# Performance work log

Measured on AMD Instinct MI355X. Metric: run time of the kernel, lower is better.

Reference implementation:

```python
import jax, jax.numpy as jnp
import numpy as np

N_NODES = 100000
N_EDGES = 1200000
IN_DIM = 256
HID = 64


def _spmm(rows, cols, vals, M):
    # sparse (COO) @ dense: gather source rows, scale by edge vals, scatter-add to dest
    gathered = M[cols] * vals[:, None]          # [E, d]
    return jax.ops.segment_sum(gathered, rows, num_segments=N_NODES)


def _gcn_embed(rows, cols, vals, X, W1, b1, W2, b2):
    # layer 1: SELU(A @ (X W1) + b1)
    Z = _spmm(rows, cols, vals, X @ W1) + b1
    Z = jax.nn.selu(Z)
    # layer 2: A @ (Z W2) + b2 (no activation)
    Z = _spmm(rows, cols, vals, Z @ W2) + b2
    # row-wise L2 normalize (F.normalize, p=2, dim=1)
    norm = jnp.sqrt(jnp.sum(Z * Z, axis=1, keepdims=True))
    return Z / jnp.maximum(norm, 1e-12)


def setup_inputs() -> dict:
    key = jax.random.key(0)
    ks = jax.random.split(key, 10)
    X1 = jax.random.normal(ks[0], (N_NODES, IN_DIM), dtype=jnp.float32)
    X2 = jax.random.normal(ks[1], (N_NODES, IN_DIM), dtype=jnp.float32)
    rows1 = jax.random.randint(ks[2], (N_EDGES,), 0, N_NODES, dtype=jnp.int32)
    cols1 = jax.random.randint(ks[3], (N_EDGES,), 0, N_NODES, dtype=jnp.int32)
    vals1 = jax.random.uniform(ks[4], (N_EDGES,), dtype=jnp.float32)
    rows2 = jax.random.randint(ks[5], (N_EDGES,), 0, N_NODES, dtype=jnp.int32)
    cols2 = jax.random.randint(ks[6], (N_EDGES,), 0, N_NODES, dtype=jnp.int32)
    vals2 = jax.random.uniform(ks[7], (N_EDGES,), dtype=jnp.float32)
    # Xavier-uniform weights, zero biases (reset_parameters)
    lim1 = float(np.sqrt(6.0 / (IN_DIM + HID)))
    lim2 = float(np.sqrt(6.0 / (HID + HID)))
    W1 = jax.random.uniform(ks[8], (IN_DIM, HID), dtype=jnp.float32, minval=-lim1, maxval=lim1)
    W2 = jax.random.uniform(ks[9], (HID, HID), dtype=jnp.float32, minval=-lim2, maxval=lim2)
    b1 = jnp.zeros((HID,), dtype=jnp.float32)
    b2 = jnp.zeros((HID,), dtype=jnp.float32)
    return {"X1": X1, "X2": X2, "rows1": rows1, "cols1": cols1, "vals1": vals1,
            "rows2": rows2, "cols2": cols2, "vals2": vals2,
            "W1": W1, "b1": b1, "W2": W2, "b2": b2}


def reference(X1, X2, rows1, cols1, vals1, rows2, cols2, vals2, W1, b1, W2, b2):
    Z1 = _gcn_embed(rows1, cols1, vals1, X1, W1, b1, W2, b2)
    Z2 = _gcn_embed(rows2, cols2, vals2, X2, W1, b1, W2, b2)
    return (Z1, Z2)
```

## Files before the change

kernel.cpp:

```cpp
#include <hip/hip_runtime.h>
#include <hip/hip_bf16.h>


#define RPB 512
#define EPB 4096
#define MAXB 8192

typedef __attribute__((ext_vector_type(8))) short short8;
typedef __attribute__((ext_vector_type(4))) short short4v;
typedef __attribute__((ext_vector_type(4))) float f32x4;

__device__ __forceinline__ float selu_f(float x) {
    const float scale = 1.0507009873554805f;
    const float alpha = 1.6732632423543772f;
    return x > 0.0f ? scale * x : scale * alpha * (__expf(x) - 1.0f);
}

__device__ __forceinline__ short f2bf(float x) {
    unsigned u = __float_as_uint(x);
    u += 0x7FFF + ((u >> 16) & 1);
    return (short)(u >> 16);
}
__device__ __forceinline__ float bf2f(short h) {
    return __uint_as_float(((unsigned)(unsigned short)h) << 16);
}

__global__ void scan_a(const int* __restrict__ counts, int* __restrict__ offs,
                       int* __restrict__ partials, int N) {
    __shared__ int sh[256];
    int tid = threadIdx.x;
    int base = blockIdx.x * 1024 + tid * 4;
    int4 c = make_int4(0, 0, 0, 0);
    if (base + 3 < N) {
        c = *(const int4*)(counts + base);
    } else {
        if (base + 0 < N) c.x = counts[base + 0];
        if (base + 1 < N) c.y = counts[base + 1];
        if (base + 2 < N) c.z = counts[base + 2];
        if (base + 3 < N) c.w = counts[base + 3];
    }
    int tsum = c.x + c.y + c.z + c.w;
    sh[tid] = tsum;
    __syncthreads();
    int val = tsum;
    for (int d = 1; d < 256; d <<= 1) {
        int t = (tid >= d) ? sh[tid - d] : 0;
        __syncthreads();
        val += t;
        sh[tid] = val;
        __syncthreads();
    }
    int excl = val - tsum;
    int4 o;
    o.x = excl; o.y = o.x + c.x; o.z = o.y + c.y; o.w = o.z + c.z;
    if (base + 3 < N) {
        *(int4*)(offs + base) = o;
    } else {
        if (base + 0 < N) offs[base + 0] = o.x;
        if (base + 1 < N) offs[base + 1] = o.y;
        if (base + 2 < N) offs[base + 2] = o.z;
        if (base + 3 < N) offs[base + 3] = o.w;
    }
    if (tid == 255) partials[blockIdx.x] = val;
}

__global__ void scan_b(int* __restrict__ partials, int nb) {
    __shared__ int sh[128];
    int tid = threadIdx.x;
    int v = (tid < nb) ? partials[tid] : 0;
    sh[tid] = v;
    __syncthreads();
    int val = v;
    for (int d = 1; d < 128; d <<= 1) {
        int t = (tid >= d) ? sh[tid - d] : 0;
        __syncthreads();
        val += t;
        sh[tid] = val;
        __syncthreads();
    }
    if (tid < nb) partials[tid] = val - v;
}

__global__ void scan_c(int* __restrict__ offs, const int* __restrict__ partials,
                       int N, int E) {
    int tid = threadIdx.x;
    int base = blockIdx.x * 1024 + tid * 4;
    int add = partials[blockIdx.x];
    if (base + 3 < N) {
        int4 o = *(int4*)(offs + base);
        o.x += add; o.y += add; o.z += add; o.w += add;
        *(int4*)(offs + base) = o;
    } else {
        for (int t = 0; t < 4; t++)
            if (base + t < N) offs[base + t] += add;
    }
    if (blockIdx.x == 0 && tid == 0) offs[N] = E;
}

__global__ __launch_bounds__(256) void bucket_hist(const int* __restrict__ rows,
                                                   int* __restrict__ cntT,
                                                   int E, int nbA, int NB) {
    __shared__ int cnt[256];
    int tid = threadIdx.x;
    cnt[tid] = 0;
    __syncthreads();
    int e0 = blockIdx.x * EPB;
#pragma unroll
    for (int k = 0; k < EPB / 256; k++) {
        int e = e0 + k * 256 + tid;
        if (e < E) atomicAdd(&cnt[rows[e] >> 9], 1);
    }
    __syncthreads();
    if (tid < NB) cntT[tid * nbA + blockIdx.x] = cnt[tid];
}

__global__ __launch_bounds__(256) void coarse_scatter(const int* __restrict__ rows,
                                                      const int* __restrict__ cols,
                                                      const float* __restrict__ vals,
                                                      const int* __restrict__ csOffs,
                                                      int2* __restrict__ ecvA,
                                                      int E, int nbA, int NB) {
    __shared__ int cnt[256];
    __shared__ int loc[256];
    __shared__ int gof[256];
    __shared__ int dstBase[EPB];
    __shared__ int2 eLDS[EPB];
    int tid = threadIdx.x, blk = blockIdx.x;
    int e0 = blk * EPB;
    cnt[tid] = 0;
    __syncthreads();
#pragma unroll
    for (int k = 0; k < EPB / 256; k++) {
        int e = e0 + k * 256 + tid;
        if (e < E) atomicAdd(&cnt[rows[e] >> 9], 1);
    }
    __syncthreads();
    int my = cnt[tid];
    loc[tid] = my;
    __syncthreads();
    int val = my;
    for (int d = 1; d < 256; d <<= 1) {
        int t = (tid >= d) ? loc[tid - d] : 0;
        __syncthreads();
        val += t;
        loc[tid] = val;
        __syncthreads();
    }
    int excl = val - my;
    loc[tid] = excl;
    cnt[tid] = excl;
    gof[tid] = (tid < NB) ? csOffs[tid * nbA + blk] : 0;
    __syncthreads();
#pragma unroll
    for (int k = 0; k < EPB / 256; k++) {
        int e = e0 + k * 256 + tid;
        if (e < E) {
            int r = rows[e];
            int b = r >> 9;
            int p = atomicAdd(&cnt[b], 1);
            eLDS[p] = make_int2(((r & (RPB - 1)) << 17) | cols[e],
                                __float_as_int(vals[e]));
            dstBase[p] = gof[b] - loc[b];
        }
    }
    __syncthreads();
    int nE = min(EPB, E - e0);
    for (int j = tid; j < nE; j += 256)
        ecvA[dstBase[j] + j] = eLDS[j];
}

__global__ __launch_bounds__(256) void fine_sort(const int* __restrict__ csOffs,
                                                 const int2* __restrict__ ecvA,
                                                 int2* __restrict__ ecv,
                                                 int* __restrict__ offs,
                                                 int nbA, int N, int E) {
    __shared__ int rcnt[RPB], roff[RPB], rcur[RPB];
    __shared__ int sh[256];
    __shared__ int2 eLDS[MAXB];
    int b = blockIdx.x, tid = threadIdx.x;
    int bs = csOffs[b * nbA];
    int be = csOffs[(b + 1) * nbA];
    int cntE = be - bs;
    if (cntE > MAXB) cntE = MAXB;
    rcnt[tid] = 0;
    rcnt[tid + 256] = 0;
    __syncthreads();
    for (int j = tid; j < cntE; j += 256)
        atomicAdd(&rcnt[ecvA[bs + j].x >> 17], 1);
    __syncthreads();
    int a0 = rcnt[2 * tid], a1 = rcnt[2 * tid + 1];
    int ps = a0 + a1;
    sh[tid] = ps;
    __syncthreads();
    int val = ps;
    for (int d = 1; d < 256; d <<= 1) {
        int t = (tid >= d) ? sh[tid - d] : 0;
        __syncthreads();
        val += t;
        sh[tid] = val;
        __syncthreads();
    }
    int exclPair = val - ps;
    roff[2 * tid] = exclPair;
    roff[2 * tid + 1] = exclPair + a0;
    rcur[2 * tid] = exclPair;
    rcur[2 * tid + 1] = exclPair + a0;
    __syncthreads();
    int row0 = b * RPB;
    for (int t2 = tid; t2 < RPB; t2 += 256) {
        int row = row0 + t2;
        if (row <= N) offs[row] = bs + roff[t2];
    }
    if (b == 0 && tid == 0) offs[N] = E;
    for (int j = tid; j < cntE; j += 256) {
        int2 p = ecvA[bs + j];
        int pos = atomicAdd(&rcur[p.x >> 17], 1);
        if (pos < MAXB) eLDS[pos] = make_int2(p.x & 0x1FFFF, p.y);
    }
    __syncthreads();
    for (int j = tid; j < cntE; j += 256)
        ecv[bs + j] = eLDS[j];
}

__global__ void prep_w(const float* __restrict__ W, short* __restrict__ th,
                       short* __restrict__ tl, int K) {
    int idx = blockIdx.x * 256 + threadIdx.x;
    if (idx < K * 64) {
        int k = idx >> 6, n = idx & 63;
        float x = W[idx];
        short h = f2bf(x);
        short l = f2bf(x - bf2f(h));
        th[n * K + k] = h;
        tl[n * K + k] = l;
    }
}

template<int K>
__global__ __launch_bounds__(256) void gemm_mfma(const float* __restrict__ A,
                                                 const short* __restrict__ Wth,
                                                 const short* __restrict__ Wtl,
                                                 float* __restrict__ C, int M) {
    constexpr int NC = K / 64;
    __shared__ short Ah[64 * 72], Al[64 * 72];
    __shared__ short Wh[64 * 72], Wl[64 * 72];
    int tid = threadIdx.x;
    int wave = tid >> 6, lane = tid & 63;
    int m = lane & 15, q = lane >> 4;
    int row0 = blockIdx.x * 64;
    int ai = tid >> 4;
    int aj = (tid & 15) * 4;
    f32x4 acc[4] = {{0.f, 0.f, 0.f, 0.f}, {0.f, 0.f, 0.f, 0.f},
                    {0.f, 0.f, 0.f, 0.f}, {0.f, 0.f, 0.f, 0.f}};

    float4 ga[4];
#pragma unroll
    for (int v = 0; v < 4; v++) {
        int gr = row0 + v * 16 + ai;
        ga[v] = make_float4(0.f, 0.f, 0.f, 0.f);
        if (gr < M) ga[v] = *(const float4*)(A + (size_t)gr * K + aj);
    }

#pragma unroll
    for (int c = 0; c < NC; c++) {
        short4v whv[4], wlv[4];
#pragma unroll
        for (int v = 0; v < 4; v++) {
            size_t wo = (size_t)(v * 16 + ai) * K + c * 64 + aj;
            whv[v] = *(const short4v*)(Wth + wo);
            wlv[v] = *(const short4v*)(Wtl + wo);
        }
        float4 gan[4];
        if (c + 1 < NC) {
#pragma unroll
            for (int v = 0; v < 4; v++) {
                int gr = row0 + v * 16 + ai;
                gan[v] = make_float4(0.f, 0.f, 0.f, 0.f);
                if (gr < M)
                    gan[v] = *(const float4*)(A + (size_t)gr * K + (c + 1) * 64 + aj);
            }
        }
#pragma unroll
        for (int v = 0; v < 4; v++) {
            int r = v * 16 + ai;
            float f[4] = {ga[v].x, ga[v].y, ga[v].z, ga[v].w};
            short4v h, l;
#pragma unroll
            for (int j = 0; j < 4; j++) {
                short hh = f2bf(f[j]);
                h[j] = hh;
                l[j] = f2bf(f[j] - bf2f(hh));
            }
            *(short4v*)(&Ah[r * 72 + aj]) = h;
            *(short4v*)(&Al[r * 72 + aj]) = l;
        }
#pragma unroll
        for (int v = 0; v < 4; v++) {
            int n = v * 16 + ai;
            *(short4v*)(&Wh[n * 72 + aj]) = whv[v];
            *(short4v*)(&Wl[n * 72 + aj]) = wlv[v];
        }
        __syncthreads();
        int ar = (16 * wave + m) * 72;
        short8 ah0 = *(const short8*)(&Ah[ar + q * 8]);
        short8 ah1 = *(const short8*)(&Ah[ar + 32 + q * 8]);
        short8 al0 = *(const short8*)(&Al[ar + q * 8]);
        short8 al1 = *(const short8*)(&Al[ar + 32 + q * 8]);
#pragma unroll
        for (int nt = 0; nt < 4; nt++) {
            int nb = (nt * 16 + m) * 72;
            short8 bh0 = *(const short8*)(&Wh[nb + q * 8]);
            short8 bh1 = *(const short8*)(&Wh[nb + 32 + q * 8]);
            short8 bl0 = *(const short8*)(&Wl[nb + q * 8]);
            short8 bl1 = *(const short8*)(&Wl[nb + 32 + q * 8]);
            acc[nt] = __builtin_amdgcn_mfma_f32_16x16x32_bf16(ah0, bh0, acc[nt], 0, 0, 0);
            acc[nt] = __builtin_amdgcn_mfma_f32_16x16x32_bf16(al0, bh0, acc[nt], 0, 0, 0);
            acc[nt] = __builtin_amdgcn_mfma_f32_16x16x32_bf16(ah0, bl0, acc[nt], 0, 0, 0);
            acc[nt] = __builtin_amdgcn_mfma_f32_16x16x32_bf16(ah1, bh1, acc[nt], 0, 0, 0);
            acc[nt] = __builtin_amdgcn_mfma_f32_16x16x32_bf16(al1, bh1, acc[nt], 0, 0, 0);
            acc[nt] = __builtin_amdgcn_mfma_f32_16x16x32_bf16(ah1, bl1, acc[nt], 0, 0, 0);
        }
        if (c + 1 < NC) {
            __syncthreads();
#pragma unroll
            for (int v = 0; v < 4; v++) ga[v] = gan[v];
        }
    }
#pragma unroll
    for (int nt = 0; nt < 4; nt++) {
#pragma unroll
        for (int r = 0; r < 4; r++) {
            int grow = row0 + 16 * wave + q * 4 + r;
            if (grow < M) C[(size_t)grow * 64 + nt * 16 + m] = acc[nt][r];
        }
    }
}

__device__ __forceinline__ void spmm_row4(const int* __restrict__ offs,
                                          const int2* __restrict__ ecv,
                                          const float* __restrict__ H,
                                          int row, int g, int f4,
                                          float& ax, float& ay, float& az, float& aw) {
    int s = offs[row], e = offs[row + 1];
    s = __builtin_amdgcn_readfirstlane(s);
    e = __builtin_amdgcn_readfirstlane(e);
    ax = ay = az = aw = 0.f;
    for (int i = s; i < e; i += 8) {
        int i0 = i + g, i1 = i + 4 + g;
        int2 p0 = ecv[i0 < e ? i0 : (e - 1)];
        int2 p1 = ecv[i1 < e ? i1 : (e - 1)];
        float v0 = (i0 < e) ? __int_as_float(p0.y) : 0.f;
        float v1 = (i1 < e) ? __int_as_float(p1.y) : 0.f;
        float4 h0 = *(const float4*)(H + (size_t)p0.x * 64 + f4);
        float4 h1 = *(const float4*)(H + (size_t)p1.x * 64 + f4);
        ax = fmaf(v0, h0.x, ax); ay = fmaf(v0, h0.y, ay);
        az = fmaf(v0, h0.z, az); aw = fmaf(v0, h0.w, aw);
        ax = fmaf(v1, h1.x, ax); ay = fmaf(v1, h1.y, ay);
        az = fmaf(v1, h1.z, az); aw = fmaf(v1, h1.w, aw);
    }
#pragma unroll
    for (int d = 16; d <= 32; d <<= 1) {
        ax += __shfl_xor(ax, d, 64);
        ay += __shfl_xor(ay, d, 64);
        az += __shfl_xor(az, d, 64);
        aw += __shfl_xor(aw, d, 64);
    }
}

__global__ __launch_bounds__(256) void spmm_selu(const int* __restrict__ offs,
                                                 const int2* __restrict__ ecv,
                                                 const float* __restrict__ H,
                                                 const float* __restrict__ bias,
                                                 float* __restrict__ out, int N) {
    int row = blockIdx.x * 4 + (threadIdx.x >> 6);
    if (row >= N) return;
    int lane = threadIdx.x & 63;
    int g = lane >> 4, f4 = (lane & 15) * 4;
    float ax, ay, az, aw;
    spmm_row4(offs, ecv, H, row, g, f4, ax, ay, az, aw);
    float4 b = *(const float4*)(bias + f4);
    if (g == 0) {
        float4 o;
        o.x = selu_f(ax + b.x);
        o.y = selu_f(ay + b.y);
        o.z = selu_f(az + b.z);
        o.w = selu_f(aw + b.w);
        *(float4*)(out + (size_t)row * 64 + f4) = o;
    }
}

__global__ __launch_bounds__(256) void spmm_norm(const int* __restrict__ offs,
                                                 const int2* __restrict__ ecv,
                                                 const float* __restrict__ H,
                                                 const float* __restrict__ bias,
                                                 float* __restrict__ out, int N) {
    int row = blockIdx.x * 4 + (threadIdx.x >> 6);
    if (row >= N) return;
    int lane = threadIdx.x & 63;
    int g = lane >> 4, f4 = (lane & 15) * 4;
    float ax, ay, az, aw;
    spmm_row4(offs, ecv, H, row, g, f4, ax, ay, az, aw);
    float4 b = *(const float4*)(bias + f4);
    float zx = ax + b.x, zy = ay + b.y, zz = az + b.z, zw = aw + b.w;
    float s2 = zx * zx + zy * zy + zz * zz + zw * zw;
#pragma unroll
    for (int d = 1; d <= 8; d <<= 1) s2 += __shfl_xor(s2, d, 64);
    float inv = 1.0f / fmaxf(sqrtf(s2), 1e-12f);
    if (g == 0) {
        float4 o;
        o.x = zx * inv; o.y = zy * inv; o.z = zz * inv; o.w = zw * inv;
        *(float4*)(out + (size_t)row * 64 + f4) = o;
    }
}

extern "C" void kernel_launch(void* const* d_in, const int* in_sizes, int n_in,
                              void* d_out, int out_size, void* d_ws, size_t ws_size,
                              hipStream_t stream) {
    const int IN_DIM = 256, HID = 64;
    const int N = in_sizes[0] / IN_DIM;
    const int E = in_sizes[2];

    const float* X[2]    = {(const float*)d_in[0], (const float*)d_in[1]};
    const int*   rows[2] = {(const int*)d_in[2], (const int*)d_in[5]};
    const int*   cols[2] = {(const int*)d_in[3], (const int*)d_in[6]};
    const float* vals[2] = {(const float*)d_in[4], (const float*)d_in[7]};
    const float* W1 = (const float*)d_in[8];
    const float* b1 = (const float*)d_in[9];
    const float* W2 = (const float*)d_in[10];
    const float* b2 = (const float*)d_in[11];
    float* out = (float*)d_out;

    const int NB  = (N + RPB - 1) / RPB;
    const int nbA = (E + EPB - 1) / EPB;
    const int M   = NB * nbA;
    const int nbScanM = (M + 1023) / 1024;
    const int nbGemm = (N + 63) / 64;
    const int nbRow  = (N + 3) / 4;

    auto align16 = [](char* p) { return (char*)(((uintptr_t)p + 15) & ~(uintptr_t)15); };
    char* w = (char*)d_ws;
    float* bufA   = (float*)w; w += (size_t)N * HID * sizeof(float);
    float* bufB   = (float*)w; w += (size_t)N * HID * sizeof(float);
    w = align16(w);
    int2*  ecv    = (int2*)w;  w += (size_t)E * sizeof(int2);
    w = align16(w);
    int*   cntT   = (int*)w;   w += (size_t)M * sizeof(int);
    w = align16(w);
    int*   csOffs = (int*)w;   w += (size_t)(M + 1) * sizeof(int);
    w = align16(w);
    int*   offs   = (int*)w;   w += (size_t)(N + 1) * sizeof(int);
    w = align16(w);
    int*   partials = (int*)w; w += 1024;
    w = align16(w);
    short* w1th = (short*)w;   w += (size_t)64 * IN_DIM * sizeof(short);
    short* w1tl = (short*)w;   w += (size_t)64 * IN_DIM * sizeof(short);
    short* w2th = (short*)w;   w += (size_t)64 * HID * sizeof(short);
    short* w2tl = (short*)w;   w += (size_t)64 * HID * sizeof(short);
    int2*  ecvA = (int2*)bufA;

    prep_w<<<(IN_DIM * 64 + 255) / 256, 256, 0, stream>>>(W1, w1th, w1tl, IN_DIM);
    prep_w<<<(HID * 64 + 255) / 256, 256, 0, stream>>>(W2, w2th, w2tl, HID);

    for (int g = 0; g < 2; g++) {
        bucket_hist<<<nbA, 256, 0, stream>>>(rows[g], cntT, E, nbA, NB);
        scan_a<<<nbScanM, 256, 0, stream>>>(cntT, csOffs, partials, M);
        scan_b<<<1, 128, 0, stream>>>(partials, nbScanM);
        scan_c<<<nbScanM, 256, 0, stream>>>(csOffs, partials, M, E);
        coarse_scatter<<<nbA, 256, 0, stream>>>(rows[g], cols[g], vals[g], csOffs,
                                                ecvA, E, nbA, NB);
        fine_sort<<<NB, 256, 0, stream>>>(csOffs, ecvA, ecv, offs, nbA, N, E);
        gemm_mfma<256><<<nbGemm, 256, 0, stream>>>(X[g], w1th, w1tl, bufA, N);
        spmm_selu<<<nbRow, 256, 0, stream>>>(offs, ecv, bufA, b1, bufB, N);
        gemm_mfma<64><<<nbGemm, 256, 0, stream>>>(bufB, w2th, w2tl, bufA, N);
        spmm_norm<<<nbRow, 256, 0, stream>>>(offs, ecv, bufA, b2,
                                             out + (size_t)g * N * HID, N);
    }
}
```

Measured before the change: 599.0 us.

## Batch both graphs into single launches via blockIdx.y and merge weight prep

Each pipeline stage (histogram, scans, scatter, sort, GEMMs, SpMMs) now processes both graphs in one launch, using a second grid dimension that selects per-graph pointers and offsets into workspace buffers that are doubled in size. The two weight-prep kernels are fused into one. This halves the kernel launch count and doubles the grid size per launch, which reduces launch gaps and fills the GPU better on the small scan and sort kernels. The cost is twice the workspace memory and larger working sets per launch, which may reduce cache locality.

```diff
diff --git a/kernel.cpp b/kernel.cpp
--- a/kernel.cpp
+++ b/kernel.cpp
@@ -25,8 +25,11 @@
     return __uint_as_float(((unsigned)(unsigned short)h) << 16);
 }
 
-__global__ void scan_a(const int* __restrict__ counts, int* __restrict__ offs,
-                       int* __restrict__ partials, int N) {
+__global__ void scan_a(const int* __restrict__ countsB, int* __restrict__ offsB,
+                       int* __restrict__ partialsB, int N) {
+    const int* counts = countsB + (size_t)blockIdx.y * N;
+    int* offs = offsB + (size_t)blockIdx.y * (N + 1);
+    int* partials = partialsB + (size_t)blockIdx.y * 512;
     __shared__ int sh[256];
     int tid = threadIdx.x;
     int base = blockIdx.x * 1024 + tid * 4;
@@ -64,7 +67,8 @@
     if (tid == 255) partials[blockIdx.x] = val;
 }
 
-__global__ void scan_b(int* __restrict__ partials, int nb) {
+__global__ void scan_b(int* __restrict__ partialsB, int nb) {
+    int* partials = partialsB + (size_t)blockIdx.y * 512;
     __shared__ int sh[128];
     int tid = threadIdx.x;
     int v = (tid < nb) ? partials[tid] : 0;
@@ -81,8 +85,10 @@
     if (tid < nb) partials[tid] = val - v;
 }
 
-__global__ void scan_c(int* __restrict__ offs, const int* __restrict__ partials,
+__global__ void scan_c(int* __restrict__ offsB, const int* __restrict__ partialsB,
                        int N, int E) {
+    int* offs = offsB + (size_t)blockIdx.y * (N + 1);
+    const int* partials = partialsB + (size_t)blockIdx.y * 512;
     int tid = threadIdx.x;
     int base = blockIdx.x * 1024 + tid * 4;
     int add = partials[blockIdx.x];
@@ -97,9 +103,12 @@
     if (blockIdx.x == 0 && tid == 0) offs[N] = E;
 }
 
-__global__ __launch_bounds__(256) void bucket_hist(const int* __restrict__ rows,
-                                                   int* __restrict__ cntT,
-                                                   int E, int nbA, int NB) {
+__global__ __launch_bounds__(256) void bucket_hist(const int* __restrict__ r0,
+                                                   const int* __restrict__ r1,
+                                                   int* __restrict__ cntTB,
+                                                   int E, int nbA, int NB, int M) {
+    const int* rows = blockIdx.y ? r1 : r0;
+    int* cntT = cntTB + (size_t)blockIdx.y * M;
     __shared__ int cnt[256];
     int tid = threadIdx.x;
     cnt[tid] = 0;
@@ -114,12 +123,20 @@
     if (tid < NB) cntT[tid * nbA + blockIdx.x] = cnt[tid];
 }
 
-__global__ __launch_bounds__(256) void coarse_scatter(const int* __restrict__ rows,
-                                                      const int* __restrict__ cols,
-                                                      const float* __restrict__ vals,
-                                                      const int* __restrict__ csOffs,
-                                                      int2* __restrict__ ecvA,
-                                                      int E, int nbA, int NB) {
+__global__ __launch_bounds__(256) void coarse_scatter(const int* __restrict__ r0,
+                                                      const int* __restrict__ r1,
+                                                      const int* __restrict__ c0,
+                                                      const int* __restrict__ c1,
+                                                      const float* __restrict__ v0,
+                                                      const float* __restrict__ v1,
+                                                      const int* __restrict__ csOffsB,
+                                                      int2* __restrict__ ecvAB,
+                                                      int E, int nbA, int NB, int M) {
+    const int* rows = blockIdx.y ? r1 : r0;
+    const int* cols = blockIdx.y ? c1 : c0;
+    const float* vals = blockIdx.y ? v1 : v0;
+    const int* csOffs = csOffsB + (size_t)blockIdx.y * (M + 1);
+    int2* ecvA = ecvAB + (size_t)blockIdx.y * E;
     __shared__ int cnt[256];
     __shared__ int loc[256];
     __shared__ int gof[256];
@@ -169,11 +186,15 @@
         ecvA[dstBase[j] + j] = eLDS[j];
 }
 
-__global__ __launch_bounds__(256) void fine_sort(const int* __restrict__ csOffs,
-                                                 const int2* __restrict__ ecvA,
-                                                 int2* __restrict__ ecv,
-                                                 int* __restrict__ offs,
-                                                 int nbA, int N, int E) {
+__global__ __launch_bounds__(256) void fine_sort(const int* __restrict__ csOffsB,
+                                                 const int2* __restrict__ ecvAB,
+                                                 int2* __restrict__ ecvB,
+                                                 int* __restrict__ offsB,
+                                                 int nbA, int N, int E, int M) {
+    const int* csOffs = csOffsB + (size_t)blockIdx.y * (M + 1);
+    const int2* ecvA = ecvAB + (size_t)blockIdx.y * E;
+    int2* ecv = ecvB + (size_t)blockIdx.y * E;
+    int* offs = offsB + (size_t)blockIdx.y * (N + 1);
     __shared__ int rcnt[RPB], roff[RPB], rcur[RPB];
     __shared__ int sh[256];
     __shared__ int2 eLDS[MAXB];
@@ -222,25 +243,40 @@
         ecv[bs + j] = eLDS[j];
 }
 
-__global__ void prep_w(const float* __restrict__ W, short* __restrict__ th,
-                       short* __restrict__ tl, int K) {
+__global__ void prep_w2(const float* __restrict__ W1, short* __restrict__ th1,
+                        short* __restrict__ tl1,
+                        const float* __restrict__ W2, short* __restrict__ th2,
+                        short* __restrict__ tl2) {
     int idx = blockIdx.x * 256 + threadIdx.x;
-    if (idx < K * 64) {
+    const int n1 = 256 * 64;
+    if (idx < n1) {
         int k = idx >> 6, n = idx & 63;
-        float x = W[idx];
+        float x = W1[idx];
         short h = f2bf(x);
         short l = f2bf(x - bf2f(h));
-        th[n * K + k] = h;
-        tl[n * K + k] = l;
+        th1[n * 256 + k] = h;
+        tl1[n * 256 + k] = l;
+    } else if (idx - n1 < 64 * 64) {
+        int i2 = idx - n1;
+        int k = i2 >> 6, n = i2 & 63;
+        float x = W2[i2];
+        short h = f2bf(x);
+        short l = f2bf(x - bf2f(h));
+        th2[n * 64 + k] = h;
+        tl2[n * 64 + k] = l;
     }
 }
 
 template<int K>
-__global__ __launch_bounds__(256) void gemm_mfma(const float* __restrict__ A,
+__global__ __launch_bounds__(256) void gemm_mfma(const float* __restrict__ A0,
+                                                 const float* __restrict__ A1,
                                                  const short* __restrict__ Wth,
                                                  const short* __restrict__ Wtl,
-                                                 float* __restrict__ C, int M) {
+                                                 float* __restrict__ C0,
+                                                 float* __restrict__ C1, int M) {
     constexpr int NC = K / 64;
+    const float* A = blockIdx.y ? A1 : A0;
+    float* C = blockIdx.y ? C1 : C0;
     __shared__ short Ah[64 * 72], Al[64 * 72];
     __shared__ short Wh[64 * 72], Wl[64 * 72];
     int tid = threadIdx.x;
@@ -366,11 +402,17 @@
     }
 }
 
-__global__ __launch_bounds__(256) void spmm_selu(const int* __restrict__ offs,
-                                                 const int2* __restrict__ ecv,
-                                                 const float* __restrict__ H,
+__global__ __launch_bounds__(256) void spmm_selu(const int* __restrict__ offsB,
+                                                 const int2* __restrict__ ecvB,
+                                                 const float* __restrict__ HB,
                                                  const float* __restrict__ bias,
-                                                 float* __restrict__ out, int N) {
+                                                 float* __restrict__ outB,
+                                                 int N, int E) {
+    int gph = blockIdx.y;
+    const int* offs = offsB + (size_t)gph * (N + 1);
+    const int2* ecv = ecvB + (size_t)gph * E;
+    const float* H = HB + (size_t)gph * N * 64;
+    float* out = outB + (size_t)gph * N * 64;
     int row = blockIdx.x * 4 + (threadIdx.x >> 6);
     if (row >= N) return;
     int lane = threadIdx.x & 63;
@@ -388,11 +430,17 @@
     }
 }
 
-__global__ __launch_bounds__(256) void spmm_norm(const int* __restrict__ offs,
-                                                 const int2* __restrict__ ecv,
-                                                 const float* __restrict__ H,
+__global__ __launch_bounds__(256) void spmm_norm(const int* __restrict__ offsB,
+                                                 const int2* __restrict__ ecvB,
+                                                 const float* __restrict__ HB,
                                                  const float* __restrict__ bias,
-                                                 float* __restrict__ out, int N) {
+                                                 float* __restrict__ outB,
+                                                 int N, int E) {
+    int gph = blockIdx.y;
+    const int* offs = offsB + (size_t)gph * (N + 1);
+    const int2* ecv = ecvB + (size_t)gph * E;
+    const float* H = HB + (size_t)gph * N * 64;
+    float* out = outB + (size_t)gph * N * 64;
     int row = blockIdx.x * 4 + (threadIdx.x >> 6);
     if (row >= N) return;
     int lane = threadIdx.x & 63;
@@ -419,10 +467,14 @@
     const int N = in_sizes[0] / IN_DIM;
     const int E = in_sizes[2];
 
-    const float* X[2]    = {(const float*)d_in[0], (const float*)d_in[1]};
-    const int*   rows[2] = {(const int*)d_in[2], (const int*)d_in[5]};
-    const int*   cols[2] = {(const int*)d_in[3], (const int*)d_in[6]};
-    const float* vals[2] = {(const float*)d_in[4], (const float*)d_in[7]};
+    const float* X1 = (const float*)d_in[0];
+    const float* X2 = (const float*)d_in[1];
+    const int*   r0 = (const int*)d_in[2];
+    const int*   c0 = (const int*)d_in[3];
+    const float* v0 = (const float*)d_in[4];
+    const int*   r1 = (const int*)d_in[5];
+    const int*   c1 = (const int*)d_in[6];
+    const float* v1 = (const float*)d_in[7];
     const float* W1 = (const float*)d_in[8];
     const float* b1 = (const float*)d_in[9];
     const float* W2 = (const float*)d_in[10];
@@ -438,18 +490,18 @@
 
     auto align16 = [](char* p) { return (char*)(((uintptr_t)p + 15) & ~(uintptr_t)15); };
     char* w = (char*)d_ws;
-    float* bufA   = (float*)w; w += (size_t)N * HID * sizeof(float);
-    float* bufB   = (float*)w; w += (size_t)N * HID * sizeof(float);
+    float* bufA   = (float*)w; w += (size_t)2 * N * HID * sizeof(float);
+    float* bufB   = (float*)w; w += (size_t)2 * N * HID * sizeof(float);
     w = align16(w);
-    int2*  ecv    = (int2*)w;  w += (size_t)E * sizeof(int2);
+    int2*  ecv    = (int2*)w;  w += (size_t)2 * E * sizeof(int2);
     w = align16(w);
-    int*   cntT   = (int*)w;   w += (size_t)M * sizeof(int);
+    int*   cntT   = (int*)w;   w += (size_t)2 * M * sizeof(int);
     w = align16(w);
-    int*   csOffs = (int*)w;   w += (size_t)(M + 1) * sizeof(int);
+    int*   csOffs = (int*)w;   w += (size_t)2 * (M + 1) * sizeof(int);
     w = align16(w);
-    int*   offs   = (int*)w;   w += (size_t)(N + 1) * sizeof(int);
+    int*   offs   = (int*)w;   w += (size_t)2 * (N + 1) * sizeof(int);
     w = align16(w);
-    int*   partials = (int*)w; w += 1024;
+    int*   partials = (int*)w; w += 2 * 512 * sizeof(int);
     w = align16(w);
     short* w1th = (short*)w;   w += (size_t)64 * IN_DIM * sizeof(short);
     short* w1tl = (short*)w;   w += (size_t)64 * IN_DIM * sizeof(short);
@@ -457,21 +509,22 @@
     short* w2tl = (short*)w;   w += (size_t)64 * HID * sizeof(short);
     int2*  ecvA = (int2*)bufA;
 
-    prep_w<<<(IN_DIM * 64 + 255) / 256, 256, 0, stream>>>(W1, w1th, w1tl, IN_DIM);
-    prep_w<<<(HID * 64 + 255) / 256, 256, 0, stream>>>(W2, w2th, w2tl, HID);
-
-    for (int g = 0; g < 2; g++) {
-        bucket_hist<<<nbA, 256, 0, stream>>>(rows[g], cntT, E, nbA, NB);
-        scan_a<<<nbScanM, 256, 0, stream>>>(cntT, csOffs, partials, M);
-        scan_b<<<1, 128, 0, stream>>>(partials, nbScanM);
-        scan_c<<<nbScanM, 256, 0, stream>>>(csOffs, partials, M, E);
-        coarse_scatter<<<nbA, 256, 0, stream>>>(rows[g], cols[g], vals[g], csOffs,
-                                                ecvA, E, nbA, NB);
-        fine_sort<<<NB, 256, 0, stream>>>(csOffs, ecvA, ecv, offs, nbA, N, E);
-        gemm_mfma<256><<<nbGemm, 256, 0, stream>>>(X[g], w1th, w1tl, bufA, N);
-        spmm_selu<<<nbRow, 256, 0, stream>>>(offs, ecv, bufA, b1, bufB, N);
-        gemm_mfma<64><<<nbGemm, 256, 0, stream>>>(bufB, w2th, w2tl, bufA, N);
-        spmm_norm<<<nbRow, 256, 0, stream>>>(offs, ecv, bufA, b2,
-                                             out + (size_t)g * N * HID, N);
-    }
-}
+    prep_w2<<<(IN_DIM * 64 + HID * 64 + 255) / 256, 256, 0, stream>>>(
+        W1, w1th, w1tl, W2, w2th, w2tl);
+
+    bucket_hist<<<dim3(nbA, 2), 256, 0, stream>>>(r0, r1, cntT, E, nbA, NB, M);
+    scan_a<<<dim3(nbScanM, 2), 256, 0, stream>>>(cntT, csOffs, partials, M);
+    scan_b<<<dim3(1, 2), 128, 0, stream>>>(partials, nbScanM);
+    scan_c<<<dim3(nbScanM, 2), 256, 0, stream>>>(csOffs, partials, M, E);
+    coarse_scatter<<<dim3(nbA, 2), 256, 0, stream>>>(r0, r1, c0, c1, v0, v1,
+                                                     csOffs, ecvA, E, nbA, NB, M);
+    fine_sort<<<dim3(NB, 2), 256, 0, stream>>>(csOffs, ecvA, ecv, offs, nbA, N, E, M);
+
+    gemm_mfma<256><<<dim3(nbGemm, 2), 256, 0, stream>>>(
+        X1, X2, w1th, w1tl, bufA, bufA + (size_t)N * HID, N);
+    spmm_selu<<<dim3(nbRow, 2), 256, 0, stream>>>(offs, ecv, bufA, b1, bufB, N, E);
+
+    gemm_mfma<64><<<dim3(nbGemm, 2), 256, 0, stream>>>(
+        bufB, bufB + (size_t)N * HID, w2th, w2tl, bufA, bufA + (size_t)N * HID, N);
+    spmm_norm<<<dim3(nbRow, 2), 256, 0, stream>>>(offs, ecv, bufA, b2, out, N, E);
+}
```

After: 537.6 us. -10.3%, faster.
